# Performance work log

Measured on AMD Instinct MI355X. Metric: run time of the kernel, lower is better.

The kernel has to match this reference:

```python
import jax, jax.numpy as jnp
import numpy as np

N = 50000
E = 800000
IN_CH = 512
OUT_CH = 64
ITERATIONS = 3  # adjacency power order; iterations-1 spmm steps


def setup_inputs() -> dict:
    key = jax.random.key(0)
    k1, k2, k3, k4, k5 = jax.random.split(key, 5)
    adj_indices = jax.random.randint(k1, (2, E), 0, N, dtype=jnp.int32)
    adj_values = jax.random.uniform(k2, (E,), dtype=jnp.float32)
    features = jax.random.normal(k3, (N, IN_CH), dtype=jnp.float32)
    # xavier-uniform init bounds
    bw = float(np.sqrt(6.0 / (IN_CH + OUT_CH)))
    weight = jax.random.uniform(k4, (IN_CH, OUT_CH), minval=-bw, maxval=bw, dtype=jnp.float32)
    bb = float(np.sqrt(6.0 / (1 + OUT_CH)))
    bias = jax.random.uniform(k5, (1, OUT_CH), minval=-bb, maxval=bb, dtype=jnp.float32)
    return {"adj_indices": adj_indices, "adj_values": adj_values,
            "features": features, "weight": weight, "bias": bias}


def reference(adj_indices, adj_values, features, weight, bias):
    # dense projection: [N, in] @ [in, out] -> [N, out]
    x = features @ weight
    # dropout is identity in eval mode (training=False)
    row, col = adj_indices[0], adj_indices[1]
    # (iterations - 1) sparse-dense matmuls: x <- A @ x
    for _ in range(ITERATIONS - 1):
        gathered = adj_values[:, None] * x[col]          # [E, out]
        x = jax.ops.segment_sum(gathered, row, num_segments=N)
    return x + bias
```

## Files before the change

kernel.cpp:

```cpp
#include <hip/hip_runtime.h>
#include <hip/hip_bf16.h>
#include <hip/hip_fp16.h>

#define NN 50000
#define INCH 512
#define OUTCH 64
#define NTILES 3125
#define MAXD 96

typedef __attribute__((ext_vector_type(8))) short short8;
typedef __attribute__((ext_vector_type(4))) float floatx4;

__device__ __forceinline__ unsigned packbf2(float a, float b) {
    __hip_bfloat162 h = __float22bfloat162_rn(make_float2(a, b));
    unsigned r;
    __builtin_memcpy(&r, &h, 4);
    return r;
}
__device__ __forceinline__ unsigned short f2bf(float f) {
    unsigned u = __float_as_uint(f);
    return (unsigned short)((u + 0x7FFFu + ((u >> 16) & 1u)) >> 16);
}

__global__ void scatter_ell(const int* __restrict__ rows, const int* __restrict__ cols,
                            const float* __restrict__ vals, int* __restrict__ deg,
                            unsigned* __restrict__ ell, int n) {
    int e = blockIdx.x * blockDim.x + threadIdx.x;
    if (e >= n) return;
    int r = rows[e];
    int slot = atomicAdd(&deg[r], 1);
    unsigned short hv = __half_as_ushort(__float2half(vals[e]));
    if (slot < MAXD) ell[(size_t)r * MAXD + slot] = (unsigned)cols[e] | ((unsigned)hv << 16);
}

#define WSTR 520
__global__ __launch_bounds__(256) void gemm_mfma(const float* __restrict__ A,
                                                 const float* __restrict__ B,
                                                 float* __restrict__ C) {
    __shared__ unsigned short Ws[64 * WSTR];
    const int t = threadIdx.x;
    const int lane = t & 63;
    const int wave = t >> 6;

    {
        const int k2 = (t >> 4) * 2;
        const int n4 = (t & 15) * 4;
#pragma unroll
        for (int c = 0; c < 16; ++c) {
            const int k = k2 + c * 32;
            const float4 w0 = *(const float4*)(B + (k + 0) * OUTCH + n4);
            const float4 w1 = *(const float4*)(B + (k + 1) * OUTCH + n4);
            *(unsigned*)&Ws[(n4 + 0) * WSTR + k] = packbf2(w0.x, w1.x);
            *(unsigned*)&Ws[(n4 + 1) * WSTR + k] = packbf2(w0.y, w1.y);
            *(unsigned*)&Ws[(n4 + 2) * WSTR + k] = packbf2(w0.z, w1.z);
            *(unsigned*)&Ws[(n4 + 3) * WSTR + k] = packbf2(w0.w, w1.w);
        }
    }
    __syncthreads();

    const int tile = blockIdx.x * 4 + wave;
    if (tile >= NTILES) return;
    const int rbase = tile * 16;
    const int frow = lane & 15;
    const int quad = lane >> 4;
    const float* Ap = A + (size_t)(rbase + frow) * INCH + quad * 8;

    floatx4 acc[4] = {floatx4{0,0,0,0}, floatx4{0,0,0,0}, floatx4{0,0,0,0}, floatx4{0,0,0,0}};

    float4 a0 = *(const float4*)(Ap);
    float4 a1 = *(const float4*)(Ap + 4);
    for (int c = 0; c < 16; ++c) {
        const float4 c0 = a0, c1 = a1;
        if (c < 15) {
            const float* An = Ap + (c + 1) * 32;
            a0 = *(const float4*)(An);
            a1 = *(const float4*)(An + 4);
        }
        uint4 au;
        au.x = packbf2(c0.x, c0.y);
        au.y = packbf2(c0.z, c0.w);
        au.z = packbf2(c1.x, c1.y);
        au.w = packbf2(c1.z, c1.w);
        const short8 af = *(const short8*)&au;
        const int koff = c * 32 + quad * 8;
#pragma unroll
        for (int f = 0; f < 4; ++f) {
            const short8 bfr = *(const short8*)&Ws[(f * 16 + frow) * WSTR + koff];
            acc[f] = __builtin_amdgcn_mfma_f32_16x16x32_bf16(af, bfr, acc[f], 0, 0, 0);
        }
    }

#pragma unroll
    for (int f = 0; f < 4; ++f) {
#pragma unroll
        for (int reg = 0; reg < 4; ++reg) {
            C[(size_t)(rbase + quad * 4 + reg) * OUTCH + f * 16 + frow] = acc[f][reg];
        }
    }
}

__global__ __launch_bounds__(256) void spmm_ell(const int* __restrict__ deg,
                                                const unsigned* __restrict__ ell,
                                                const float* __restrict__ xin,
                                                float* __restrict__ xout,
                                                const float* __restrict__ bias) {
    const int t = threadIdx.x;
    const int lane = t & 63;
    const int eslot = lane >> 4;
    const int c4 = (lane & 15) * 4;
    const int row = blockIdx.x * 4 + (t >> 6);
    const int d = deg[row];
    const unsigned* ebase = ell + (size_t)row * MAXD;
    float4 acc = make_float4(0.f, 0.f, 0.f, 0.f);
    for (int i = eslot; i < d; i += 4) {
        const unsigned p = ebase[i];
        const float4 x = *(const float4*)(xin + (size_t)(p & 0xFFFFu) * OUTCH + c4);
        const float v = __half2float(__ushort_as_half((unsigned short)(p >> 16)));
        acc.x = fmaf(v, x.x, acc.x); acc.y = fmaf(v, x.y, acc.y);
        acc.z = fmaf(v, x.z, acc.z); acc.w = fmaf(v, x.w, acc.w);
    }
    acc.x += __shfl_xor(acc.x, 16, 64); acc.y += __shfl_xor(acc.y, 16, 64);
    acc.z += __shfl_xor(acc.z, 16, 64); acc.w += __shfl_xor(acc.w, 16, 64);
    acc.x += __shfl_xor(acc.x, 32, 64); acc.y += __shfl_xor(acc.y, 32, 64);
    acc.z += __shfl_xor(acc.z, 32, 64); acc.w += __shfl_xor(acc.w, 32, 64);
    if (eslot == 0) {
        if (bias) {
            const float4 bv = *(const float4*)(bias + c4);
            acc.x += bv.x; acc.y += bv.y; acc.z += bv.z; acc.w += bv.w;
        }
        *(float4*)(xout + (size_t)row * OUTCH + c4) = acc;
    }
}

extern "C" void kernel_launch(void* const* d_in, const int* in_sizes, int n_in,
                              void* d_out, int out_size, void* d_ws, size_t ws_size,
                              hipStream_t stream) {
    const int*   adj   = (const int*)d_in[0];
    const float* avals = (const float*)d_in[1];
    const float* feat  = (const float*)d_in[2];
    const float* W     = (const float*)d_in[3];
    const float* bias  = (const float*)d_in[4];
    float* out = (float*)d_out;

    const int E_ = in_sizes[1];
    const int* rows = adj;
    const int* cols = adj + E_;

    float*    x0   = (float*)d_ws;
    float*    x1   = x0 + (size_t)NN * OUTCH;
    unsigned* ell  = (unsigned*)(x1 + (size_t)NN * OUTCH);
    int*      deg  = (int*)(ell + (size_t)NN * MAXD);

    hipMemsetAsync(deg, 0, NN * sizeof(int), stream);
    scatter_ell<<<(E_ + 255) / 256, 256, 0, stream>>>(rows, cols, avals, deg, ell, E_);

    gemm_mfma<<<(NTILES + 3) / 4, 256, 0, stream>>>(feat, W, x0);

    spmm_ell<<<NN / 4, 256, 0, stream>>>(deg, ell, x0, x1, nullptr);
    spmm_ell<<<NN / 4, 256, 0, stream>>>(deg, ell, x1, out, bias);
}
```

Baseline: 284.7 us.

## Store intermediate features in bf16 and fuse ELL scatter into GEMM launch

Intermediate projected features and the first SpMM output are stored as bf16 instead of fp32, halving gather traffic in the sparse matmuls. The edge-to-ELL scatter kernel is merged into the GEMM launch as extra blocks, so adjacency construction overlaps the dense projection and one launch is removed. Rounding intermediates to bf16 adds precision loss across two propagation steps.

```diff
diff --git a/kernel.cpp b/kernel.cpp
--- a/kernel.cpp
+++ b/kernel.cpp
@@ -7,6 +7,8 @@
 #define OUTCH 64
 #define NTILES 3125
 #define MAXD 96
+#define GB 782
+#define SB 256
 
 typedef __attribute__((ext_vector_type(8))) short short8;
 typedef __attribute__((ext_vector_type(4))) float floatx4;
@@ -21,24 +23,31 @@
     unsigned u = __float_as_uint(f);
     return (unsigned short)((u + 0x7FFFu + ((u >> 16) & 1u)) >> 16);
 }
-
-__global__ void scatter_ell(const int* __restrict__ rows, const int* __restrict__ cols,
-                            const float* __restrict__ vals, int* __restrict__ deg,
-                            unsigned* __restrict__ ell, int n) {
-    int e = blockIdx.x * blockDim.x + threadIdx.x;
-    if (e >= n) return;
-    int r = rows[e];
-    int slot = atomicAdd(&deg[r], 1);
-    unsigned short hv = __half_as_ushort(__float2half(vals[e]));
-    if (slot < MAXD) ell[(size_t)r * MAXD + slot] = (unsigned)cols[e] | ((unsigned)hv << 16);
+__device__ __forceinline__ float bf2f(unsigned short u) {
+    return __uint_as_float(((unsigned)u) << 16);
 }
 
 #define WSTR 520
-__global__ __launch_bounds__(256) void gemm_mfma(const float* __restrict__ A,
-                                                 const float* __restrict__ B,
-                                                 float* __restrict__ C) {
+__global__ __launch_bounds__(256) void fused_gemm_scatter(
+        const float* __restrict__ A, const float* __restrict__ B,
+        unsigned short* __restrict__ C,
+        const int* __restrict__ rows, const int* __restrict__ cols,
+        const float* __restrict__ vals, int* __restrict__ deg,
+        unsigned* __restrict__ ell, int E_) {
     __shared__ unsigned short Ws[64 * WSTR];
     const int t = threadIdx.x;
+
+    if (blockIdx.x >= GB) {
+        for (int e = (blockIdx.x - GB) * 256 + t; e < E_; e += SB * 256) {
+            const int r = rows[e];
+            const int slot = atomicAdd(&deg[r], 1);
+            const unsigned short hv = __half_as_ushort(__float2half(vals[e]));
+            if (slot < MAXD)
+                ell[(size_t)r * MAXD + slot] = (unsigned)cols[e] | ((unsigned)hv << 16);
+        }
+        return;
+    }
+
     const int lane = t & 63;
     const int wave = t >> 6;
 
@@ -94,15 +103,16 @@
     for (int f = 0; f < 4; ++f) {
 #pragma unroll
         for (int reg = 0; reg < 4; ++reg) {
-            C[(size_t)(rbase + quad * 4 + reg) * OUTCH + f * 16 + frow] = acc[f][reg];
+            C[(size_t)(rbase + quad * 4 + reg) * OUTCH + f * 16 + frow] = f2bf(acc[f][reg]);
         }
     }
 }
 
+template <bool LAST>
 __global__ __launch_bounds__(256) void spmm_ell(const int* __restrict__ deg,
                                                 const unsigned* __restrict__ ell,
-                                                const float* __restrict__ xin,
-                                                float* __restrict__ xout,
+                                                const unsigned short* __restrict__ xin,
+                                                void* __restrict__ xout_,
                                                 const float* __restrict__ bias) {
     const int t = threadIdx.x;
     const int lane = t & 63;
@@ -114,21 +124,27 @@
     float4 acc = make_float4(0.f, 0.f, 0.f, 0.f);
     for (int i = eslot; i < d; i += 4) {
         const unsigned p = ebase[i];
-        const float4 x = *(const float4*)(xin + (size_t)(p & 0xFFFFu) * OUTCH + c4);
+        const ushort4 xv = *(const ushort4*)(xin + (size_t)(p & 0xFFFFu) * OUTCH + c4);
         const float v = __half2float(__ushort_as_half((unsigned short)(p >> 16)));
-        acc.x = fmaf(v, x.x, acc.x); acc.y = fmaf(v, x.y, acc.y);
-        acc.z = fmaf(v, x.z, acc.z); acc.w = fmaf(v, x.w, acc.w);
+        acc.x = fmaf(v, bf2f(xv.x), acc.x);
+        acc.y = fmaf(v, bf2f(xv.y), acc.y);
+        acc.z = fmaf(v, bf2f(xv.z), acc.z);
+        acc.w = fmaf(v, bf2f(xv.w), acc.w);
     }
     acc.x += __shfl_xor(acc.x, 16, 64); acc.y += __shfl_xor(acc.y, 16, 64);
     acc.z += __shfl_xor(acc.z, 16, 64); acc.w += __shfl_xor(acc.w, 16, 64);
     acc.x += __shfl_xor(acc.x, 32, 64); acc.y += __shfl_xor(acc.y, 32, 64);
     acc.z += __shfl_xor(acc.z, 32, 64); acc.w += __shfl_xor(acc.w, 32, 64);
     if (eslot == 0) {
-        if (bias) {
+        if (LAST) {
             const float4 bv = *(const float4*)(bias + c4);
             acc.x += bv.x; acc.y += bv.y; acc.z += bv.z; acc.w += bv.w;
+            *(float4*)((float*)xout_ + (size_t)row * OUTCH + c4) = acc;
+        } else {
+            ushort4 o;
+            o.x = f2bf(acc.x); o.y = f2bf(acc.y); o.z = f2bf(acc.z); o.w = f2bf(acc.w);
+            *(ushort4*)((unsigned short*)xout_ + (size_t)row * OUTCH + c4) = o;
         }
-        *(float4*)(xout + (size_t)row * OUTCH + c4) = acc;
     }
 }
 
@@ -146,16 +162,16 @@
     const int* rows = adj;
     const int* cols = adj + E_;
 
-    float*    x0   = (float*)d_ws;
-    float*    x1   = x0 + (size_t)NN * OUTCH;
-    unsigned* ell  = (unsigned*)(x1 + (size_t)NN * OUTCH);
-    int*      deg  = (int*)(ell + (size_t)NN * MAXD);
+    unsigned short* x0 = (unsigned short*)d_ws;
+    unsigned short* x1 = x0 + (size_t)NN * OUTCH;
+    unsigned* ell = (unsigned*)(x1 + (size_t)NN * OUTCH);
+    int* deg = (int*)(ell + (size_t)NN * MAXD);
 
     hipMemsetAsync(deg, 0, NN * sizeof(int), stream);
-    scatter_ell<<<(E_ + 255) / 256, 256, 0, stream>>>(rows, cols, avals, deg, ell, E_);
 
-    gemm_mfma<<<(NTILES + 3) / 4, 256, 0, stream>>>(feat, W, x0);
+    fused_gemm_scatter<<<GB + SB, 256, 0, stream>>>(feat, W, x0, rows, cols, avals,
+                                                    deg, ell, E_);
 
-    spmm_ell<<<NN / 4, 256, 0, stream>>>(deg, ell, x0, x1, nullptr);
-    spmm_ell<<<NN / 4, 256, 0, stream>>>(deg, ell, x1, out, bias);
+    spmm_ell<false><<<NN / 4, 256, 0, stream>>>(deg, ell, x0, x1, nullptr);
+    spmm_ell<true><<<NN / 4, 256, 0, stream>>>(deg, ell, x1, out, bias);
 }
```

Result: faster. 271.3 us (-4.7%).
